# Kernel tuning notes

Measured on AMD Instinct MI355X. Metric: run time of the kernel, lower is better.

The kernel has to match this reference:

```python
import jax, jax.numpy as jnp
import numpy as np

N_NODES = 50000

def setup_inputs() -> dict:
    key = jax.random.key(0)
    ks = jax.random.split(key, 8)
    input_dim, hidden_dim, output_dim = 128, 256, 64
    x = jax.random.normal(ks[0], (N_NODES, input_dim), dtype=jnp.float32)
    edge_index = jax.random.randint(ks[1], (2, 800000), 0, N_NODES, dtype=jnp.int64)
    s1 = 1.0 / np.sqrt(input_dim)
    s2 = 1.0 / np.sqrt(hidden_dim)
    W1 = jax.random.uniform(ks[2], (input_dim, hidden_dim), jnp.float32, -s1, s1)
    b1 = jax.random.uniform(ks[3], (hidden_dim,), jnp.float32, -s1, s1)
    W2 = jax.random.uniform(ks[4], (hidden_dim, hidden_dim), jnp.float32, -s2, s2)
    b2 = jax.random.uniform(ks[5], (hidden_dim,), jnp.float32, -s2, s2)
    Wc = jax.random.uniform(ks[6], (hidden_dim, output_dim), jnp.float32, -s2, s2)
    bc = jax.random.uniform(ks[7], (output_dim,), jnp.float32, -s2, s2)
    return {"x": x, "edge_index": edge_index, "W1": W1, "b1": b1,
            "W2": W2, "b2": b2, "Wc": Wc, "bc": bc}

def reference(x, edge_index, W1, b1, W2, b2, Wc, bc):
    src, dst = edge_index[0], edge_index[1]
    # GINConv (eps=0): h_i = (1+eps)*x_i + sum_{j->i} x_j
    aggr = jax.ops.segment_sum(x[src], dst, num_segments=N_NODES)  # [N, d_in]
    h = x + aggr
    # 2-layer MLP: Linear -> ReLU -> Linear
    h = jax.nn.relu(h @ W1 + b1) @ W2 + b2  # [N, hidden]
    # classifier on ReLU(conv output)
    return jax.nn.relu(h) @ Wc + bc  # [N, out]
```

## Files before the change

### kernel.cpp

```cpp
#include <hip/hip_runtime.h>
#include <hip/hip_bf16.h>

#define N_NODES 50000
#define M_PAD   50048
#define N_EDGES 800000
#define NBUCK   391
#define NB_EB8  196
#define NB_CAST 3125
#define NB_TR   448
#define EBMAX   4096

typedef __bf16 bf16x8 __attribute__((ext_vector_type(8)));
typedef float  f32x4  __attribute__((ext_vector_type(4)));

__device__ __forceinline__ ushort f2bf(float f) {
    __hip_bfloat16 h = __float2bfloat16(f);
    return __builtin_bit_cast(ushort, h);
}
__device__ __forceinline__ float bf2f(ushort u) {
    return __builtin_bit_cast(float, (unsigned)u << 16);
}

__device__ __forceinline__ void gload16(const ushort* g, ushort* l) {
    __builtin_amdgcn_global_load_lds(
        (const __attribute__((address_space(1))) unsigned*)g,
        (__attribute__((address_space(3))) unsigned*)l, 16, 0, 0);
}

__device__ __forceinline__ void transpose_one(const float* W, ushort* WT,
                                              int K, int N, int t) {
    int k = t / N, n = t % N;
    WT[n * K + k] = f2bf(W[t]);
}

__global__ __launch_bounds__(256) void k_prep(const float* __restrict__ x,
                                              ushort* __restrict__ xb,
                                              const float* __restrict__ W1, ushort* __restrict__ W1T,
                                              const float* __restrict__ W2, ushort* __restrict__ W2T,
                                              const float* __restrict__ Wc, ushort* __restrict__ WcT,
                                              int* __restrict__ bcur) {
    int b = blockIdx.x, t = threadIdx.x;
    if (b < NB_CAST) {
        int i = b * 256 + t;
        const float4* x4 = (const float4*)x;
        float4 a = x4[(size_t)i * 2], bb = x4[(size_t)i * 2 + 1];
        ushort o[8];
        o[0] = f2bf(a.x); o[1] = f2bf(a.y); o[2] = f2bf(a.z); o[3] = f2bf(a.w);
        o[4] = f2bf(bb.x); o[5] = f2bf(bb.y); o[6] = f2bf(bb.z); o[7] = f2bf(bb.w);
        *(uint4*)(xb + (size_t)i * 8) = *(uint4*)o;
    } else if (b < NB_CAST + NB_TR) {
        int tg = (b - NB_CAST) * 256 + t;
        const int S1 = 128 * 256, S2 = 256 * 256, S3 = 256 * 64;
        if (tg < S1) transpose_one(W1, W1T, 128, 256, tg);
        else if (tg < S1 + S2) transpose_one(W2, W2T, 256, 256, tg - S1);
        else if (tg < S1 + S2 + S3) transpose_one(Wc, WcT, 256, 64, tg - S1 - S2);
    } else {
        for (int i = t; i < 400; i += 256) bcur[i] = 0;
    }
}

__global__ __launch_bounds__(512) void k_bscatter(const int* __restrict__ ei,
                                                  int* __restrict__ bcur,
                                                  unsigned* __restrict__ pbuf) {
    __shared__ int lh[NBUCK];
    __shared__ int lbase[NBUCK];
    int t = threadIdx.x;
    for (int i = t; i < NBUCK; i += 512) lh[i] = 0;
    __syncthreads();
    int base = blockIdx.x * 4096 + t;
    int s[8], bk[8], rk[8], lo[8];
#pragma unroll
    for (int k = 0; k < 8; ++k) {
        int e = base + k * 512;
        bool ok = e < N_EDGES;
        int ee = ok ? e : 0;
        s[k] = ei[ee];
        int d = ei[N_EDGES + ee];
        bk[k] = ok ? (d >> 7) : -1;
        lo[k] = d & 127;
    }
#pragma unroll
    for (int k = 0; k < 8; ++k)
        if (bk[k] >= 0) rk[k] = atomicAdd(&lh[bk[k]], 1);
    __syncthreads();
    for (int i = t; i < NBUCK; i += 512) {
        int v = lh[i];
        lbase[i] = v ? atomicAdd(&bcur[i], v) : 0;
    }
    __syncthreads();
#pragma unroll
    for (int k = 0; k < 8; ++k)
        if (bk[k] >= 0) {
            int pos = lbase[bk[k]] + rk[k];
            if (pos < EBMAX)
                pbuf[bk[k] * EBMAX + pos] = (unsigned)s[k] | ((unsigned)lo[k] << 17);
        }
}

__global__ __launch_bounds__(256) void k_bplace(const unsigned* __restrict__ pbuf,
                                                const int* __restrict__ bcur,
                                                int* __restrict__ nodestart,
                                                int* __restrict__ nodecnt,
                                                int* __restrict__ elist) {
    __shared__ int lcnt[128], lexc[128], lcur[128];
    int b = blockIdx.x, t = threadIdx.x;
    int m = bcur[b]; if (m > EBMAX) m = EBMAX;
    const unsigned* pb = pbuf + b * EBMAX;
    if (t < 128) lcnt[t] = 0;
    __syncthreads();
    for (int i = t; i < m; i += 256)
        atomicAdd(&lcnt[pb[i] >> 17], 1);
    __syncthreads();
    if (t < 128) lexc[t] = lcnt[t];
    __syncthreads();
#pragma unroll
    for (int off = 1; off < 128; off <<= 1) {
        int u = (t < 128 && t >= off) ? lexc[t - off] : 0;
        __syncthreads();
        if (t < 128) lexc[t] += u;
        __syncthreads();
    }
    if (t < 128) {
        int e = lexc[t] - lcnt[t];
        int node = (b << 7) + t;
        if (node < N_NODES) {
            nodestart[node] = b * EBMAX + e;
            nodecnt[node] = lcnt[t];
        }
        lcur[t] = e;
    }
    __syncthreads();
    for (int i = t; i < m; i += 256) {
        unsigned pr = pb[i];
        int pos = atomicAdd(&lcur[pr >> 17], 1);
        elist[b * EBMAX + pos] = (int)(pr & 0x1FFFF);
    }
}

__global__ __launch_bounds__(256) void k_aggregate(const ushort* __restrict__ xb,
                                                   const int* __restrict__ nodestart,
                                                   const int* __restrict__ nodecnt,
                                                   const int* __restrict__ elist,
                                                   ushort* __restrict__ hsum) {
    int g = threadIdx.x >> 5, lane = threadIdx.x & 31;
    int node = blockIdx.x * 8 + g;
    if (node >= N_NODES) return;
    const ushort4* x4 = (const ushort4*)xb;
    ushort4 mine = x4[(size_t)node * 32 + lane];
    float acc0 = bf2f(mine.x), acc1 = bf2f(mine.y), acc2 = bf2f(mine.z), acc3 = bf2f(mine.w);
    int beg = nodestart[node], cnt = nodecnt[node];
    for (int base = 0; base < cnt; base += 32) {
        int mrem = cnt - base;
        int idx = (lane < mrem) ? elist[beg + base + lane] : 0;
        int c = mrem < 32 ? mrem : 32;
        for (int j = 0; j < c; j += 16) {
            ushort4 v[16];
#pragma unroll
            for (int u = 0; u < 16; ++u) {
                bool ok = (j + u) < c;
                if (ok) {
                    int s = __shfl(idx, j + u, 32);
                    v[u] = x4[(size_t)s * 32 + lane];
                } else {
                    v[u] = make_ushort4(0, 0, 0, 0);
                }
            }
#pragma unroll
            for (int u = 0; u < 16; ++u) {
                acc0 += bf2f(v[u].x); acc1 += bf2f(v[u].y);
                acc2 += bf2f(v[u].z); acc3 += bf2f(v[u].w);
            }
        }
    }
    ushort4 o;
    o.x = f2bf(acc0); o.y = f2bf(acc1); o.z = f2bf(acc2); o.w = f2bf(acc3);
    *(ushort4*)(hsum + (size_t)node * 128 + lane * 4) = o;
}

__global__ __launch_bounds__(512) void k_mlp3(const ushort* __restrict__ hsum,
                                              const ushort* __restrict__ W1T,
                                              const float* __restrict__ b1,
                                              const ushort* __restrict__ W2T,
                                              const float* __restrict__ b2,
                                              const ushort* __restrict__ WcT,
                                              const float* __restrict__ bc,
                                              float* __restrict__ out, int M) {
    __shared__ ushort sA[64 * 64];
    __shared__ ushort sB[256 * 64];
    __shared__ ushort ht[64 * 256];

    int m0 = blockIdx.x * 64;
    int tid = threadIdx.x, wv = tid >> 6, lane = tid & 63;
    int lr = lane & 15;
    int kq = (lane >> 4) << 3;
    int l8 = (lane >> 3) & 7, c8 = lane & 7;
    int swz8 = c8 ^ l8;

    int wrow0 = (wv >> 2) * 32;
    int wcol0 = (wv & 3) * 64;
    int crow = (lane >> 4) << 2;

    f32x4 acc[2][4];

#pragma unroll
    for (int m = 0; m < 2; ++m)
#pragma unroll
        for (int n = 0; n < 4; ++n) acc[m][n] = 0;

    for (int kb = 0; kb < 128; kb += 64) {
        gload16(hsum + (size_t)(m0 + wv * 8 + l8) * 128 + kb + swz8 * 8, sA + wv * 8 * 64);
#pragma unroll
        for (int i = 0; i < 4; ++i) {
            int rg = wv * 32 + i * 8;
            gload16(W1T + (size_t)(rg + l8) * 128 + kb + swz8 * 8, sB + rg * 64);
        }
        __syncthreads();
#pragma unroll
        for (int kk = 0; kk < 64; kk += 32) {
            int cb = (kk + kq) * 2;
            bf16x8 af[2], bfr[4];
#pragma unroll
            for (int m = 0; m < 2; ++m) {
                int r = wrow0 + m * 16 + lr;
                af[m] = __builtin_bit_cast(bf16x8,
                    *(const uint4*)((const char*)sA + r * 128 + (cb ^ ((r & 7) << 4))));
            }
#pragma unroll
            for (int n = 0; n < 4; ++n) {
                int r = wcol0 + n * 16 + lr;
                bfr[n] = __builtin_bit_cast(bf16x8,
                    *(const uint4*)((const char*)sB + r * 128 + (cb ^ ((r & 7) << 4))));
            }
#pragma unroll
            for (int m = 0; m < 2; ++m)
#pragma unroll
                for (int n = 0; n < 4; ++n)
                    acc[m][n] = __builtin_amdgcn_mfma_f32_16x16x32_bf16(
                        af[m], bfr[n], acc[m][n], 0, 0, 0);
        }
        __syncthreads();
    }
#pragma unroll
    for (int n = 0; n < 4; ++n) {
        int col = wcol0 + n * 16 + lr;
        float bv = b1[col];
#pragma unroll
        for (int m = 0; m < 2; ++m) {
#pragma unroll
            for (int r = 0; r < 4; ++r) {
                int row = wrow0 + m * 16 + crow + r;
                int sc = ((((col >> 3) ^ (row & 7)) << 3) | (col & 7));
                ht[row * 256 + sc] = f2bf(fmaxf(acc[m][n][r] + bv, 0.0f));
            }
        }
    }
    __syncthreads();

#pragma unroll
    for (int m = 0; m < 2; ++m)
#pragma unroll
        for (int n = 0; n < 4; ++n) acc[m][n] = 0;

    for (int kb = 0; kb < 256; kb += 64) {
#pragma unroll
        for (int i = 0; i < 4; ++i) {
            int rg = wv * 32 + i * 8;
            gload16(W2T + (size_t)(rg + l8) * 256 + kb + swz8 * 8, sB + rg * 64);
        }
        __syncthreads();
#pragma unroll
        for (int kk = 0; kk < 64; kk += 32) {
            int cc = kb + kk + kq;
            int cb = (kk + kq) * 2;
            bf16x8 af[2], bfr[4];
#pragma unroll
            for (int m = 0; m < 2; ++m) {
                int r = wrow0 + m * 16 + lr;
                af[m] = __builtin_bit_cast(bf16x8,
                    *(const uint4*)(ht + r * 256 + ((((cc >> 3) ^ (r & 7)) << 3))));
            }
#pragma unroll
            for (int n = 0; n < 4; ++n) {
                int r = wcol0 + n * 16 + lr;
                bfr[n] = __builtin_bit_cast(bf16x8,
                    *(const uint4*)((const char*)sB + r * 128 + (cb ^ ((r & 7) << 4))));
            }
#pragma unroll
            for (int m = 0; m < 2; ++m)
#pragma unroll
                for (int n = 0; n < 4; ++n)
                    acc[m][n] = __builtin_amdgcn_mfma_f32_16x16x32_bf16(
                        af[m], bfr[n], acc[m][n], 0, 0, 0);
        }
        __syncthreads();
    }
#pragma unroll
    for (int n = 0; n < 4; ++n) {
        int col = wcol0 + n * 16 + lr;
        float bv = b2[col];
#pragma unroll
        for (int m = 0; m < 2; ++m) {
#pragma unroll
            for (int r = 0; r < 4; ++r) {
                int row = wrow0 + m * 16 + crow + r;
                int sc = ((((col >> 3) ^ (row & 7)) << 3) | (col & 7));
                ht[row * 256 + sc] = f2bf(fmaxf(acc[m][n][r] + bv, 0.0f));
            }
        }
    }
#pragma unroll
    for (int i = 0; i < 4; ++i)
        gload16(WcT + (size_t)(wv * 8 + l8) * 256 + i * 64 + swz8 * 8,
                sB + i * 4096 + wv * 8 * 64);
    __syncthreads();

    f32x4 acc3[2];
#pragma unroll
    for (int n = 0; n < 2; ++n) acc3[n] = 0;
    int mrow0 = (wv & 3) * 16;
    int ncol0 = (wv >> 2) * 32;
    int arow3 = mrow0 + lr;
#pragma unroll
    for (int kb4 = 0; kb4 < 4; ++kb4) {
#pragma unroll
        for (int kk = 0; kk < 64; kk += 32) {
            int cc = kb4 * 64 + kk + kq;
            int cb = (kk + kq) * 2;
            bf16x8 a = __builtin_bit_cast(bf16x8,
                *(const uint4*)(ht + arow3 * 256 + ((((cc >> 3) ^ (arow3 & 7)) << 3))));
#pragma unroll
            for (int n = 0; n < 2; ++n) {
                int r = ncol0 + n * 16 + lr;
                bf16x8 b = __builtin_bit_cast(bf16x8,
                    *(const uint4*)((const char*)sB + kb4 * 8192 + r * 128 +
                                    (cb ^ ((r & 7) << 4))));
                acc3[n] = __builtin_amdgcn_mfma_f32_16x16x32_bf16(a, b, acc3[n], 0, 0, 0);
            }
        }
    }
#pragma unroll
    for (int n = 0; n < 2; ++n) {
        int col = ncol0 + n * 16 + lr;
        float bv = bc[col];
#pragma unroll
        for (int r = 0; r < 4; ++r) {
            int grow = m0 + mrow0 + crow + r;
            if (grow < M) out[(size_t)grow * 64 + col] = acc3[n][r] + bv;
        }
    }
}


extern "C" void kernel_launch(void* const* d_in, const int* in_sizes, int n_in,
                              void* d_out, int out_size, void* d_ws, size_t ws_size,
                              hipStream_t stream) {
    const float* x  = (const float*)d_in[0];
    const int*   ei = (const int*)d_in[1];
    const float* W1 = (const float*)d_in[2];
    const float* b1 = (const float*)d_in[3];
    const float* W2 = (const float*)d_in[4];
    const float* b2 = (const float*)d_in[5];
    const float* Wc = (const float*)d_in[6];
    const float* bc = (const float*)d_in[7];
    float* out = (float*)d_out;

    char* p = (char*)d_ws;
    int* bcur        = (int*)p; p += 400 * 4;
    int* nodestart   = (int*)p; p += M_PAD * 4;
    int* nodecnt     = (int*)p; p += M_PAD * 4;
    unsigned* pbuf   = (unsigned*)p; p += (size_t)NBUCK * EBMAX * 4;
    int* elist       = (int*)p; p += (size_t)NBUCK * EBMAX * 4;
    ushort* W1T = (ushort*)p; p += 256 * 128 * 2;
    ushort* W2T = (ushort*)p; p += 256 * 256 * 2;
    ushort* WcT = (ushort*)p; p += 64 * 256 * 2;
    ushort* xb  = (ushort*)p; p += (size_t)N_NODES * 128 * 2;
    ushort* hsum = (ushort*)p; p += (size_t)M_PAD * 128 * 2;

    k_prep<<<NB_CAST + NB_TR + 1, 256, 0, stream>>>(x, xb, W1, W1T, W2, W2T, Wc, WcT, bcur);
    k_bscatter<<<NB_EB8, 512, 0, stream>>>(ei, bcur, pbuf);
    k_bplace<<<NBUCK, 256, 0, stream>>>(pbuf, bcur, nodestart, nodecnt, elist);
    k_aggregate<<<(N_NODES + 7) / 8, 256, 0, stream>>>(xb, nodestart, nodecnt, elist, hsum);
    k_mlp3<<<M_PAD / 64, 512, 0, stream>>>(hsum, W1T, b1, W2T, b2, WcT, bc, out, N_NODES);
}
```

Measured before the change: 102.3 us.

## Fuse neighbor aggregation into the MLP kernel, writing aggregated rows to LDS

Merges the gather-sum aggregation kernel into the 3-layer MLP kernel. Each 64-node block now gathers neighbor rows with 16-lane groups and writes the bf16 sums straight into swizzled shared memory instead of a global hsum buffer. Both halves of W1T are prefetched into LDS (one half into the ht buffer), so the first GEMM runs without the per-k-slice reload and sync. This drops one kernel launch and the hsum global write and read. In exchange only 782 blocks do the irregular gather, with less parallelism and latency hiding than the old 6250-block aggregate kernel.

```diff
diff --git a/kernel.cpp b/kernel.cpp
--- a/kernel.cpp
+++ b/kernel.cpp
@@ -137,55 +137,18 @@
     }
 }
 
-__global__ __launch_bounds__(256) void k_aggregate(const ushort* __restrict__ xb,
-                                                   const int* __restrict__ nodestart,
-                                                   const int* __restrict__ nodecnt,
-                                                   const int* __restrict__ elist,
-                                                   ushort* __restrict__ hsum) {
-    int g = threadIdx.x >> 5, lane = threadIdx.x & 31;
-    int node = blockIdx.x * 8 + g;
-    if (node >= N_NODES) return;
-    const ushort4* x4 = (const ushort4*)xb;
-    ushort4 mine = x4[(size_t)node * 32 + lane];
-    float acc0 = bf2f(mine.x), acc1 = bf2f(mine.y), acc2 = bf2f(mine.z), acc3 = bf2f(mine.w);
-    int beg = nodestart[node], cnt = nodecnt[node];
-    for (int base = 0; base < cnt; base += 32) {
-        int mrem = cnt - base;
-        int idx = (lane < mrem) ? elist[beg + base + lane] : 0;
-        int c = mrem < 32 ? mrem : 32;
-        for (int j = 0; j < c; j += 16) {
-            ushort4 v[16];
-#pragma unroll
-            for (int u = 0; u < 16; ++u) {
-                bool ok = (j + u) < c;
-                if (ok) {
-                    int s = __shfl(idx, j + u, 32);
-                    v[u] = x4[(size_t)s * 32 + lane];
-                } else {
-                    v[u] = make_ushort4(0, 0, 0, 0);
-                }
-            }
-#pragma unroll
-            for (int u = 0; u < 16; ++u) {
-                acc0 += bf2f(v[u].x); acc1 += bf2f(v[u].y);
-                acc2 += bf2f(v[u].z); acc3 += bf2f(v[u].w);
-            }
-        }
-    }
-    ushort4 o;
-    o.x = f2bf(acc0); o.y = f2bf(acc1); o.z = f2bf(acc2); o.w = f2bf(acc3);
-    *(ushort4*)(hsum + (size_t)node * 128 + lane * 4) = o;
-}
-
-__global__ __launch_bounds__(512) void k_mlp3(const ushort* __restrict__ hsum,
-                                              const ushort* __restrict__ W1T,
-                                              const float* __restrict__ b1,
-                                              const ushort* __restrict__ W2T,
-                                              const float* __restrict__ b2,
-                                              const ushort* __restrict__ WcT,
-                                              const float* __restrict__ bc,
-                                              float* __restrict__ out, int M) {
-    __shared__ ushort sA[64 * 64];
+__global__ __launch_bounds__(512) void k_fused(const ushort* __restrict__ xb,
+                                               const int* __restrict__ nodestart,
+                                               const int* __restrict__ nodecnt,
+                                               const int* __restrict__ elist,
+                                               const ushort* __restrict__ W1T,
+                                               const float* __restrict__ b1,
+                                               const ushort* __restrict__ W2T,
+                                               const float* __restrict__ b2,
+                                               const ushort* __restrict__ WcT,
+                                               const float* __restrict__ bc,
+                                               float* __restrict__ out, int M) {
+    __shared__ ushort sA[2][64 * 64];
     __shared__ ushort sB[256 * 64];
     __shared__ ushort ht[64 * 256];
 
@@ -196,6 +159,63 @@
     int l8 = (lane >> 3) & 7, c8 = lane & 7;
     int swz8 = c8 ^ l8;
 
+#pragma unroll
+    for (int i = 0; i < 4; ++i) {
+        int rg = wv * 32 + i * 8;
+        gload16(W1T + (size_t)(rg + l8) * 128 + swz8 * 8, sB + rg * 64);
+        gload16(W1T + (size_t)(rg + l8) * 128 + 64 + swz8 * 8, ht + rg * 64);
+    }
+
+    {
+        int grp = tid >> 4, l16 = tid & 15;
+        for (int nd = grp; nd < 64; nd += 32) {
+            int node = m0 + nd;
+            float a[8];
+#pragma unroll
+            for (int k = 0; k < 8; ++k) a[k] = 0.0f;
+            if (node < N_NODES) {
+                uint4 mine = *(const uint4*)(xb + (size_t)node * 128 + l16 * 8);
+                const ushort* pm = (const ushort*)&mine;
+#pragma unroll
+                for (int k = 0; k < 8; ++k) a[k] = bf2f(pm[k]);
+                int beg = nodestart[node], cnt = nodecnt[node];
+                for (int base = 0; base < cnt; base += 16) {
+                    int rem = cnt - base;
+                    int idx = (l16 < rem) ? elist[beg + base + l16] : 0;
+                    int c = rem < 16 ? rem : 16;
+                    int j = 0;
+                    for (; j + 8 <= c; j += 8) {
+                        uint4 v[8];
+#pragma unroll
+                        for (int u = 0; u < 8; ++u) {
+                            int s = __shfl(idx, j + u, 16);
+                            v[u] = *(const uint4*)(xb + (size_t)s * 128 + l16 * 8);
+                        }
+#pragma unroll
+                        for (int u = 0; u < 8; ++u) {
+                            const ushort* pv = (const ushort*)&v[u];
+#pragma unroll
+                            for (int k = 0; k < 8; ++k) a[k] += bf2f(pv[k]);
+                        }
+                    }
+                    for (; j < c; ++j) {
+                        int s = __shfl(idx, j, 16);
+                        uint4 v = *(const uint4*)(xb + (size_t)s * 128 + l16 * 8);
+                        const ushort* pv = (const ushort*)&v;
+#pragma unroll
+                        for (int k = 0; k < 8; ++k) a[k] += bf2f(pv[k]);
+                    }
+                }
+            }
+            ushort o[8];
+#pragma unroll
+            for (int k = 0; k < 8; ++k) o[k] = f2bf(a[k]);
+            int h = l16 >> 3, cch = l16 & 7;
+            *(uint4*)(&sA[h][nd * 64 + ((cch ^ (nd & 7)) << 3)]) = *(uint4*)o;
+        }
+    }
+    __syncthreads();
+
     int wrow0 = (wv >> 2) * 32;
     int wcol0 = (wv & 3) * 64;
     int crow = (lane >> 4) << 2;
@@ -207,14 +227,10 @@
 #pragma unroll
         for (int n = 0; n < 4; ++n) acc[m][n] = 0;
 
-    for (int kb = 0; kb < 128; kb += 64) {
-        gload16(hsum + (size_t)(m0 + wv * 8 + l8) * 128 + kb + swz8 * 8, sA + wv * 8 * 64);
-#pragma unroll
-        for (int i = 0; i < 4; ++i) {
-            int rg = wv * 32 + i * 8;
-            gload16(W1T + (size_t)(rg + l8) * 128 + kb + swz8 * 8, sB + rg * 64);
-        }
-        __syncthreads();
+#pragma unroll
+    for (int kbh = 0; kbh < 2; ++kbh) {
+        const ushort* asrc = sA[kbh];
+        const ushort* bsrc = kbh ? ht : sB;
 #pragma unroll
         for (int kk = 0; kk < 64; kk += 32) {
             int cb = (kk + kq) * 2;
@@ -223,13 +239,13 @@
             for (int m = 0; m < 2; ++m) {
                 int r = wrow0 + m * 16 + lr;
                 af[m] = __builtin_bit_cast(bf16x8,
-                    *(const uint4*)((const char*)sA + r * 128 + (cb ^ ((r & 7) << 4))));
+                    *(const uint4*)((const char*)asrc + r * 128 + (cb ^ ((r & 7) << 4))));
             }
 #pragma unroll
             for (int n = 0; n < 4; ++n) {
                 int r = wcol0 + n * 16 + lr;
                 bfr[n] = __builtin_bit_cast(bf16x8,
-                    *(const uint4*)((const char*)sB + r * 128 + (cb ^ ((r & 7) << 4))));
+                    *(const uint4*)((const char*)bsrc + r * 128 + (cb ^ ((r & 7) << 4))));
             }
 #pragma unroll
             for (int m = 0; m < 2; ++m)
@@ -238,8 +254,9 @@
                     acc[m][n] = __builtin_amdgcn_mfma_f32_16x16x32_bf16(
                         af[m], bfr[n], acc[m][n], 0, 0, 0);
         }
-        __syncthreads();
-    }
+    }
+    __syncthreads();
+
 #pragma unroll
     for (int n = 0; n < 4; ++n) {
         int col = wcol0 + n * 16 + lr;
@@ -374,11 +391,10 @@
     ushort* W2T = (ushort*)p; p += 256 * 256 * 2;
     ushort* WcT = (ushort*)p; p += 64 * 256 * 2;
     ushort* xb  = (ushort*)p; p += (size_t)N_NODES * 128 * 2;
-    ushort* hsum = (ushort*)p; p += (size_t)M_PAD * 128 * 2;
 
     k_prep<<<NB_CAST + NB_TR + 1, 256, 0, stream>>>(x, xb, W1, W1T, W2, W2T, Wc, WcT, bcur);
     k_bscatter<<<NB_EB8, 512, 0, stream>>>(ei, bcur, pbuf);
     k_bplace<<<NBUCK, 256, 0, stream>>>(pbuf, bcur, nodestart, nodecnt, elist);
-    k_aggregate<<<(N_NODES + 7) / 8, 256, 0, stream>>>(xb, nodestart, nodecnt, elist, hsum);
-    k_mlp3<<<M_PAD / 64, 512, 0, stream>>>(hsum, W1T, b1, W2T, b2, WcT, bc, out, N_NODES);
-}
+    k_fused<<<M_PAD / 64, 512, 0, stream>>>(xb, nodestart, nodecnt, elist,
+                                            W1T, b1, W2T, b2, WcT, bc, out, N_NODES);
+}
```

Result: faster. 96.27 us, median of 3 (-5.9%).
